# Kernel tuning notes

Hardware: AMD Instinct MI355X
Metric: run time of the kernel (lower is better)

## Reference

```python
import jax, jax.numpy as jnp
import numpy as np

M_LOCAL = 100000
N_GLOBAL = 50000
C = 128
E = 1600000
EDGE_DIM = 16
BN_EPS = 1e-5


def setup_inputs() -> dict:
    key = jax.random.key(0)
    ks = jax.random.split(key, 12)
    s = 1.0 / np.sqrt(C)
    inp = {
        "h_local": jax.random.normal(ks[0], (M_LOCAL, C), jnp.float32),
        "h_global": jax.random.normal(ks[1], (N_GLOBAL, C), jnp.float32),
        "ea_flat": jax.random.normal(ks[2], (E, EDGE_DIM), jnp.float32),
        # GIN MLP: Linear(C,C) -> ReLU -> Linear(C,C)
        "W1": jax.random.normal(ks[3], (C, C), jnp.float32) * s,
        "b1": jnp.zeros((C,), jnp.float32),
        "W2": jax.random.normal(ks[4], (C, C), jnp.float32) * s,
        "b2": jnp.zeros((C,), jnp.float32),
        "eps": jnp.zeros((), jnp.float32),  # GIN train_eps, init 0
        "gamma_l": jnp.ones((C,), jnp.float32),
        "beta_l": jnp.zeros((C,), jnp.float32),
        "gamma_g": jnp.ones((C,), jnp.float32),
        "beta_g": jnp.zeros((C,), jnp.float32),
        "intra_ei": jax.random.randint(ks[5], (2, E), 0, M_LOCAL, jnp.int32),
        "node_ids": jax.random.randint(ks[6], (M_LOCAL,), 0, N_GLOBAL, jnp.int32),
        "valid": jnp.ones((M_LOCAL,), jnp.bool_),
        "N_total": N_GLOBAL,
    }
    return inp


def _batchnorm(x, gamma, beta):
    # training-mode BN: biased batch statistics over node dim
    mu = jnp.mean(x, axis=0)
    var = jnp.mean((x - mu) ** 2, axis=0)
    return (x - mu) * jax.lax.rsqrt(var + BN_EPS) * gamma + beta


def reference(h_local, h_global, ea_flat, W1, b1, W2, b2, eps,
              gamma_l, beta_l, gamma_g, beta_g,
              intra_ei, node_ids, valid, N_total):
    M = h_local.shape[0]
    valid_f = valid.astype(h_local.dtype)[:, None]
    clamped = jnp.maximum(node_ids, 0)

    # inject global context, zero padding
    h_in = (h_local + h_global[clamped]) * valid_f

    # GINConv: mlp((1+eps)*x + sum_{j->i} x_j)   (ea_flat unused for 'gin')
    src, dst = intra_ei[0], intra_ei[1]
    agg = jax.ops.segment_sum(h_in[src], dst, num_segments=M)
    pre = (1.0 + eps) * h_in + agg
    h_local_new = jnp.maximum(pre @ W1 + b1, 0.0) @ W2 + b2
    h_local_new = h_local_new * valid_f

    # cross-subgraph consensus: scatter mean into global nodes
    h_sum = jax.ops.segment_sum(h_local_new, clamped, num_segments=N_total)
    v_cnt = jax.ops.segment_sum(valid_f[:, 0], clamped, num_segments=N_total)
    h_global_new = h_sum / jnp.maximum(v_cnt, 1.0)[:, None]

    # local track: BN + residual (Identity since in==out) + mask (dropout p=0)
    h_local_new = _batchnorm(h_local_new, gamma_l, beta_l) + h_local
    h_local_new = h_local_new * valid_f

    # global track: BN + residual
    h_global_new = _batchnorm(h_global_new, gamma_g, beta_g) + h_global

    return (h_local_new, h_global_new)
```

## Files before the change

### kernel.cpp

```cpp
#include <hip/hip_runtime.h>

#define CDIM 128
#define NBE 3125
#define NBN 391
#define CAPE 1024
#define CAPN 512
#define CHUNK 8192
#define EPB 16
#define BOE 3126
#define BON 392
#define H1LD 136

typedef __bf16 bf16x8 __attribute__((ext_vector_type(8)));
typedef __bf16 bf16x4 __attribute__((ext_vector_type(4)));
typedef float f32x4 __attribute__((ext_vector_type(4)));

__global__ __launch_bounds__(512) void k_front(
    const int* __restrict__ ei, const int* __restrict__ nid,
    int* __restrict__ packed_e, int* __restrict__ boff_e,
    int* __restrict__ packed_n, int* __restrict__ boff_n,
    const float* __restrict__ hl, const float* __restrict__ hg,
    __bf16* __restrict__ h_in,
    const float* __restrict__ W1, const float* __restrict__ W2,
    __bf16* __restrict__ Wt1, __bf16* __restrict__ Wt2,
    int E, int M, int gE, int gN, int gInit)
{
    __shared__ int lh[4096];
    __shared__ int stg[CHUNK];
    __shared__ int lp[512];
    int t = threadIdx.x;
    int bid = blockIdx.x;

    if (bid < gE) {
        int e0 = bid * CHUNK;
        int n = min(CHUNK, E - e0);
        for (int i = t; i < 4096; i += 512) lh[i] = 0;
        __syncthreads();
        int sv[EPB], dv[EPB];
#pragma unroll
        for (int k = 0; k < EPB; ++k) {
            int j = t + k * 512;
            if (j < n) {
                sv[k] = ei[e0 + j];
                dv[k] = ei[E + e0 + j];
                atomicAdd(&lh[dv[k] >> 5], 1);
            }
        }
        __syncthreads();
        int base = t * 8;
        int v[8], s = 0;
#pragma unroll
        for (int k = 0; k < 8; ++k) { v[k] = lh[base + k]; s += v[k]; }
        lp[t] = s;
        __syncthreads();
        for (int st = 1; st < 512; st <<= 1) {
            int a = (t >= st) ? lp[t - st] : 0;
            __syncthreads();
            lp[t] += a;
            __syncthreads();
        }
        int run = lp[t] - s;
#pragma unroll
        for (int k = 0; k < 8; ++k) { lh[base + k] = run; run += v[k]; }
        __syncthreads();
        int* brow = boff_e + (size_t)bid * BOE;
        for (int b = t; b < BOE; b += 512) brow[b] = lh[b];
        __syncthreads();
#pragma unroll
        for (int k = 0; k < EPB; ++k) {
            int j = t + k * 512;
            if (j < n) {
                int pos = atomicAdd(&lh[dv[k] >> 5], 1);
                stg[pos] = sv[k] | ((dv[k] & 31) << 17);
            }
        }
        __syncthreads();
        for (int j = t; j < n; j += 512) packed_e[(size_t)e0 + j] = stg[j];
    } else if (bid < gE + gN) {
        int c = bid - gE;
        int i0 = c * CHUNK;
        int n = min(CHUNK, M - i0);
        lh[t] = 0;
        __syncthreads();
        int iv[EPB], gv[EPB];
#pragma unroll
        for (int k = 0; k < EPB; ++k) {
            int j = t + k * 512;
            if (j < n) {
                iv[k] = i0 + j;
                gv[k] = max(nid[i0 + j], 0);
                atomicAdd(&lh[gv[k] >> 7], 1);
            }
        }
        __syncthreads();
        int v0 = lh[t];
        lp[t] = v0;
        __syncthreads();
        for (int st = 1; st < 512; st <<= 1) {
            int a = (t >= st) ? lp[t - st] : 0;
            __syncthreads();
            lp[t] += a;
            __syncthreads();
        }
        lh[t] = lp[t] - v0;
        __syncthreads();
        int* brow = boff_n + (size_t)c * BON;
        for (int b = t; b < BON; b += 512) brow[b] = lh[b];
        __syncthreads();
#pragma unroll
        for (int k = 0; k < EPB; ++k) {
            int j = t + k * 512;
            if (j < n) {
                int pos = atomicAdd(&lh[gv[k] >> 7], 1);
                stg[pos] = iv[k] | ((gv[k] & 127) << 17);
            }
        }
        __syncthreads();
        for (int j = t; j < n; j += 512) packed_n[(size_t)i0 + j] = stg[j];
    } else if (bid < gE + gN + gInit) {
        int idx = (bid - gE - gN) * 512 + t;
        if (idx >= M * 16) return;
        int i = idx >> 4, q8 = idx & 15;
        int g = max(nid[i], 0);
        const float4* hl4 = reinterpret_cast<const float4*>(hl);
        const float4* hg4 = reinterpret_cast<const float4*>(hg);
        float4 a0 = hl4[i * 32 + q8 * 2], a1 = hl4[i * 32 + q8 * 2 + 1];
        float4 b0 = hg4[g * 32 + q8 * 2], b1 = hg4[g * 32 + q8 * 2 + 1];
        bf16x8 o;
        o[0] = (__bf16)(a0.x + b0.x); o[1] = (__bf16)(a0.y + b0.y);
        o[2] = (__bf16)(a0.z + b0.z); o[3] = (__bf16)(a0.w + b0.w);
        o[4] = (__bf16)(a1.x + b1.x); o[5] = (__bf16)(a1.y + b1.y);
        o[6] = (__bf16)(a1.z + b1.z); o[7] = (__bf16)(a1.w + b1.w);
        *reinterpret_cast<bf16x8*>(&h_in[(size_t)i * CDIM + q8 * 8]) = o;
    } else {
        int idx = (bid - gE - gN - gInit) * 512 + t;
        int k = idx >> 7, n = idx & 127;
        Wt1[n * CDIM + k] = (__bf16)W1[k * CDIM + n];
        Wt2[n * CDIM + k] = (__bf16)W2[k * CDIM + n];
    }
}

__global__ __launch_bounds__(256) void k_agg_fused(
    const __bf16* __restrict__ h_in, const int* __restrict__ packed_e,
    const int* __restrict__ boff_e, const float* __restrict__ epsp,
    __bf16* __restrict__ pre, int M, int gE)
{
    __shared__ int lsrc[CAPE], lsrt[CAPE];
    __shared__ int lscan[256];
    __shared__ int lcnt[32], lbase[32], lpos[32];
    int t = threadIdx.x, b = blockIdx.x;
    int start = 0, len = 0;
    if (t < gE) {
        const int* brow = boff_e + (size_t)t * BOE + b;
        start = brow[0];
        len = brow[1] - start;
    }
    lscan[t] = len;
    __syncthreads();
    for (int st = 1; st < 256; st <<= 1) {
        int a = (t >= st) ? lscan[t - st] : 0;
        __syncthreads();
        lscan[t] += a;
        __syncthreads();
    }
    int myoff = lscan[t] - len;
    int ntot = min(lscan[255], CAPE);
    int cbase = (t < gE) ? t : 0;
    const int* seg = packed_e + (size_t)cbase * CHUNK + start;
    for (int k = 0; k < len; ++k) {
        int o = myoff + k;
        if (o < CAPE) lsrc[o] = seg[k];
    }
    if (t < 32) lcnt[t] = 0;
    __syncthreads();
    for (int j = t; j < ntot; j += 256) atomicAdd(&lcnt[lsrc[j] >> 17], 1);
    __syncthreads();
    if (t == 0) {
        int acc = 0;
        for (int i = 0; i < 32; ++i) { int c = lcnt[i]; lbase[i] = acc; lpos[i] = acc; acc += c; }
    }
    __syncthreads();
    for (int j = t; j < ntot; j += 256) {
        int p = lsrc[j];
        int r = atomicAdd(&lpos[p >> 17], 1);
        lsrt[r] = p & 0x1FFFF;
    }
    __syncthreads();

    float es = 1.0f + epsp[0];
    int slot = t >> 4, q = t & 15;
    int r0 = b * 32;
#pragma unroll
    for (int rr0 = 0; rr0 < 2; ++rr0) {
        int rr = slot + rr0 * 16;
        int row = r0 + rr;
        if (row >= M) break;
        bf16x8 a = *reinterpret_cast<const bf16x8*>(&h_in[(size_t)row * CDIM + q * 8]);
        float f[8];
#pragma unroll
        for (int k2 = 0; k2 < 8; ++k2) f[k2] = es * (float)a[k2];
        int sb = lbase[rr], cnt = lcnt[rr];
        int j = 0;
        for (; j + 3 < cnt; j += 4) {
            int s0 = lsrt[sb + j], s1 = lsrt[sb + j + 1];
            int s2 = lsrt[sb + j + 2], s3 = lsrt[sb + j + 3];
            bf16x8 u0 = *reinterpret_cast<const bf16x8*>(&h_in[(size_t)s0 * CDIM + q * 8]);
            bf16x8 u1 = *reinterpret_cast<const bf16x8*>(&h_in[(size_t)s1 * CDIM + q * 8]);
            bf16x8 u2 = *reinterpret_cast<const bf16x8*>(&h_in[(size_t)s2 * CDIM + q * 8]);
            bf16x8 u3 = *reinterpret_cast<const bf16x8*>(&h_in[(size_t)s3 * CDIM + q * 8]);
#pragma unroll
            for (int k2 = 0; k2 < 8; ++k2)
                f[k2] += ((float)u0[k2] + (float)u1[k2]) + ((float)u2[k2] + (float)u3[k2]);
        }
        for (; j < cnt; ++j) {
            int s0 = lsrt[sb + j];
            bf16x8 u0 = *reinterpret_cast<const bf16x8*>(&h_in[(size_t)s0 * CDIM + q * 8]);
#pragma unroll
            for (int k2 = 0; k2 < 8; ++k2) f[k2] += (float)u0[k2];
        }
        bf16x8 o;
#pragma unroll
        for (int k2 = 0; k2 < 8; ++k2) o[k2] = (__bf16)f[k2];
        *reinterpret_cast<bf16x8*>(&pre[(size_t)row * CDIM + q * 8]) = o;
    }
}

__global__ __launch_bounds__(256) void k_mlp(
    const __bf16* __restrict__ pre, const __bf16* __restrict__ Wt1,
    const __bf16* __restrict__ Wt2, const float* __restrict__ b1,
    const float* __restrict__ b2, __bf16* __restrict__ y,
    float* __restrict__ part, int M)
{
    __shared__ bf16x8 w_lds4[2048];
    __shared__ __bf16 h1t[64 * H1LD];
    __shared__ float pst[256];
    int t = threadIdx.x;
#pragma unroll
    for (int j = 0; j < 8; ++j) {
        int c = t + j * 256;
        int n = c >> 4, cr = c & 15, kc = cr >> 2, g = cr & 3;
        w_lds4[((n >> 4) * 4 + kc) * 64 + g * 16 + (n & 15)] =
            reinterpret_cast<const bf16x8*>(Wt1)[c];
    }
    if (t < 256) pst[t] = 0.f;
    __syncthreads();

    int wave = t >> 6, lane = t & 63;
    int r0 = blockIdx.x * 64 + wave * 16;
    int srcrow = min(r0 + (lane & 15), M - 1);
    int krow = (lane >> 4) * 8;
    int col = lane & 15;

    bf16x8 a[4];
#pragma unroll
    for (int kc = 0; kc < 4; ++kc)
        a[kc] = *reinterpret_cast<const bf16x8*>(
            &pre[(size_t)srcrow * CDIM + kc * 32 + krow]);

    f32x4 acc1[8] = {};
#pragma unroll
    for (int kc = 0; kc < 4; ++kc)
#pragma unroll
        for (int nt = 0; nt < 8; ++nt)
            acc1[nt] = __builtin_amdgcn_mfma_f32_16x16x32_bf16(
                a[kc], w_lds4[(nt * 4 + kc) * 64 + lane], acc1[nt], 0, 0, 0);

    int lrowb = wave * 16 + (lane >> 4) * 4;
#pragma unroll
    for (int nt = 0; nt < 8; ++nt) {
        float bv = b1[nt * 16 + col];
#pragma unroll
        for (int reg = 0; reg < 4; ++reg) {
            float v = fmaxf(acc1[nt][reg] + bv, 0.f);
            h1t[(lrowb + reg) * H1LD + nt * 16 + col] = (__bf16)v;
        }
    }
    __syncthreads();

#pragma unroll
    for (int j = 0; j < 8; ++j) {
        int c = t + j * 256;
        int n = c >> 4, cr = c & 15, kc = cr >> 2, g = cr & 3;
        w_lds4[((n >> 4) * 4 + kc) * 64 + g * 16 + (n & 15)] =
            reinterpret_cast<const bf16x8*>(Wt2)[c];
    }
    __syncthreads();

    int lrow = wave * 16 + (lane & 15);
    bf16x8 a2[4];
#pragma unroll
    for (int kc = 0; kc < 4; ++kc)
        a2[kc] = *reinterpret_cast<const bf16x8*>(&h1t[lrow * H1LD + kc * 32 + krow]);

    f32x4 acc2[8] = {};
#pragma unroll
    for (int kc = 0; kc < 4; ++kc)
#pragma unroll
        for (int nt = 0; nt < 8; ++nt)
            acc2[nt] = __builtin_amdgcn_mfma_f32_16x16x32_bf16(
                a2[kc], w_lds4[(nt * 4 + kc) * 64 + lane], acc2[nt], 0, 0, 0);

    int rowbase = r0 + (lane >> 4) * 4;
#pragma unroll
    for (int nt = 0; nt < 8; ++nt) {
        float bv = b2[nt * 16 + col];
        float s = 0.f, s2 = 0.f;
#pragma unroll
        for (int reg = 0; reg < 4; ++reg) {
            int row = rowbase + reg;
            float v = acc2[nt][reg] + bv;
            if (row < M) {
                y[(size_t)row * CDIM + nt * 16 + col] = (__bf16)v;
                s += v;
                s2 = fmaf(v, v, s2);
            }
        }
        s += __shfl_xor(s, 16); s += __shfl_xor(s, 32);
        s2 += __shfl_xor(s2, 16); s2 += __shfl_xor(s2, 32);
        if ((lane >> 4) == 0) {
            atomicAdd(&pst[nt * 16 + col], s);
            atomicAdd(&pst[128 + nt * 16 + col], s2);
        }
    }
    __syncthreads();
    if (t < 256) part[(size_t)blockIdx.x * 256 + t] = pst[t];
}

__global__ __launch_bounds__(256) void k_gmean(
    const __bf16* __restrict__ y, const int* __restrict__ packed_n,
    const int* __restrict__ boff_n, float* __restrict__ out_g,
    float* __restrict__ part, int N, int gN)
{
    __shared__ int lall[CAPN], lrows[CAPN];
    __shared__ int lscan[256];
    __shared__ int lcnt[32], lbase[32], lpos[32];
    __shared__ float pst[256];
    int t = threadIdx.x;
    int b = blockIdx.x >> 2;
    int quarter = blockIdx.x & 3;
    int start = 0, len = 0;
    if (t < gN) {
        const int* brow = boff_n + (size_t)t * BON + b;
        start = brow[0];
        len = brow[1] - start;
    }
    lscan[t] = len;
    pst[t] = 0.f;
    __syncthreads();
    for (int st = 1; st < 256; st <<= 1) {
        int a = (t >= st) ? lscan[t - st] : 0;
        __syncthreads();
        lscan[t] += a;
        __syncthreads();
    }
    int myoff = lscan[t] - len;
    int ntot = min(lscan[255], CAPN);
    int cbase = (t < gN) ? t : 0;
    const int* seg = packed_n + (size_t)cbase * CHUNK + start;
    for (int k = 0; k < len; ++k) {
        int o = myoff + k;
        if (o < CAPN) lall[o] = seg[k];
    }
    if (t < 32) lcnt[t] = 0;
    __syncthreads();
    for (int j = t; j < ntot; j += 256) {
        int ld = lall[j] >> 17;
        if ((ld >> 5) == quarter) atomicAdd(&lcnt[ld & 31], 1);
    }
    __syncthreads();
    if (t == 0) {
        int acc = 0;
        for (int i = 0; i < 32; ++i) { int c = lcnt[i]; lbase[i] = acc; lpos[i] = acc; acc += c; }
    }
    __syncthreads();
    for (int j = t; j < ntot; j += 256) {
        int p = lall[j];
        int ld = p >> 17;
        if ((ld >> 5) == quarter) {
            int r = atomicAdd(&lpos[ld & 31], 1);
            lrows[r] = p & 0x1FFFF;
        }
    }
    __syncthreads();

    int slot = t >> 4, q = t & 15;
    int g0 = b * 128 + quarter * 32;
    float csum[8] = {}, csq[8] = {};
#pragma unroll
    for (int rr0 = 0; rr0 < 2; ++rr0) {
        int rr = slot + rr0 * 16;
        int g = g0 + rr;
        if (g >= N) break;
        float f[8] = {};
        int sb = lbase[rr], cnt = lcnt[rr];
        int j = 0;
        for (; j + 1 < cnt; j += 2) {
            int ra = lrows[sb + j], rb = lrows[sb + j + 1];
            bf16x8 va = *reinterpret_cast<const bf16x8*>(&y[(size_t)ra * CDIM + q * 8]);
            bf16x8 vb = *reinterpret_cast<const bf16x8*>(&y[(size_t)rb * CDIM + q * 8]);
#pragma unroll
            for (int k2 = 0; k2 < 8; ++k2) f[k2] += (float)va[k2] + (float)vb[k2];
        }
        if (j < cnt) {
            int ra = lrows[sb + j];
            bf16x8 va = *reinterpret_cast<const bf16x8*>(&y[(size_t)ra * CDIM + q * 8]);
#pragma unroll
            for (int k2 = 0; k2 < 8; ++k2) f[k2] += (float)va[k2];
        }
        float inv = 1.0f / fmaxf((float)cnt, 1.0f);
        float4 o0, o1;
        o0.x = f[0] * inv; o0.y = f[1] * inv; o0.z = f[2] * inv; o0.w = f[3] * inv;
        o1.x = f[4] * inv; o1.y = f[5] * inv; o1.z = f[6] * inv; o1.w = f[7] * inv;
        float* dst = out_g + (size_t)g * CDIM + q * 8;
        *reinterpret_cast<float4*>(dst) = o0;
        *reinterpret_cast<float4*>(dst + 4) = o1;
        float m[8] = {o0.x, o0.y, o0.z, o0.w, o1.x, o1.y, o1.z, o1.w};
#pragma unroll
        for (int k2 = 0; k2 < 8; ++k2) {
            csum[k2] += m[k2];
            csq[k2] = fmaf(m[k2], m[k2], csq[k2]);
        }
    }
#pragma unroll
    for (int k2 = 0; k2 < 8; ++k2) {
        atomicAdd(&pst[q * 8 + k2], csum[k2]);
        atomicAdd(&pst[128 + q * 8 + k2], csq[k2]);
    }
    __syncthreads();
    if (t < 256) part[(size_t)blockIdx.x * 256 + t] = pst[t];
}

__global__ __launch_bounds__(256) void k_reduce_scale(
    const float* __restrict__ part_l, int nl,
    const float* __restrict__ part_g, int ng,
    const float* __restrict__ gl, const float* __restrict__ bl,
    const float* __restrict__ gg, const float* __restrict__ bg,
    float* __restrict__ sc, int M, int N)
{
    int c = blockIdx.x;
    bool isL = c < 128;
    const float* part = isL ? part_l : part_g;
    int n = isL ? nl : ng;
    int col = isL ? c : c - 128;
    int t = threadIdx.x;
    float s1 = 0.f, s2 = 0.f;
    for (int i = t; i < n; i += 256) {
        const float* row = part + (size_t)i * 256;
        s1 += row[col];
        s2 += row[128 + col];
    }
    __shared__ float sh1[256], sh2[256];
    sh1[t] = s1; sh2[t] = s2;
    __syncthreads();
    for (int w = 128; w > 0; w >>= 1) {
        if (t < w) { sh1[t] += sh1[t + w]; sh2[t] += sh2[t + w]; }
        __syncthreads();
    }
    if (t == 0) {
        float cnt = isL ? (float)M : (float)N;
        float mu = sh1[0] / cnt;
        float var = sh2[0] / cnt - mu * mu;
        float gamma = isL ? gl[col] : gg[col];
        float beta  = isL ? bl[col] : bg[col];
        float sca = gamma * rsqrtf(var + 1e-5f);
        int off = isL ? 0 : 256;
        sc[off + col] = sca;
        sc[off + 128 + col] = beta - mu * sca;
    }
}

__global__ __launch_bounds__(256) void k_fin(
    const __bf16* __restrict__ y, const float* __restrict__ hl,
    float* __restrict__ out_l, float* __restrict__ out_g,
    const float* __restrict__ hg, const float* __restrict__ sc,
    int M, int N, int gFinL)
{
    int bid = blockIdx.x;
    if (bid < gFinL) {
        int idx = bid * 256 + threadIdx.x;
        if (idx >= M * 32) return;
        int q = idx & 31;
        float4 s4 = reinterpret_cast<const float4*>(sc)[q];
        float4 h4 = reinterpret_cast<const float4*>(sc + 128)[q];
        bf16x4 v = *reinterpret_cast<const bf16x4*>(&y[(size_t)idx * 4]);
        float4 r = reinterpret_cast<const float4*>(hl)[idx];
        reinterpret_cast<float4*>(out_l)[idx] = make_float4(
            fmaf((float)v[0], s4.x, h4.x) + r.x, fmaf((float)v[1], s4.y, h4.y) + r.y,
            fmaf((float)v[2], s4.z, h4.z) + r.z, fmaf((float)v[3], s4.w, h4.w) + r.w);
    } else {
        int idx = (bid - gFinL) * 256 + threadIdx.x;
        if (idx >= N * 32) return;
        int q = idx & 31;
        float4 s4 = reinterpret_cast<const float4*>(sc + 256)[q];
        float4 h4 = reinterpret_cast<const float4*>(sc + 384)[q];
        float4 v = reinterpret_cast<float4*>(out_g)[idx];
        float4 r = reinterpret_cast<const float4*>(hg)[idx];
        reinterpret_cast<float4*>(out_g)[idx] = make_float4(
            fmaf(v.x, s4.x, h4.x) + r.x, fmaf(v.y, s4.y, h4.y) + r.y,
            fmaf(v.z, s4.z, h4.z) + r.z, fmaf(v.w, s4.w, h4.w) + r.w);
    }
}

extern "C" void kernel_launch(void* const* d_in, const int* in_sizes, int n_in,
                              void* d_out, int out_size, void* d_ws, size_t ws_size,
                              hipStream_t stream)
{
    const float* h_local  = (const float*)d_in[0];
    const float* h_global = (const float*)d_in[1];
    const float* W1   = (const float*)d_in[3];
    const float* b1   = (const float*)d_in[4];
    const float* W2   = (const float*)d_in[5];
    const float* b2   = (const float*)d_in[6];
    const float* eps  = (const float*)d_in[7];
    const float* gl   = (const float*)d_in[8];
    const float* bl   = (const float*)d_in[9];
    const float* gg   = (const float*)d_in[10];
    const float* bg   = (const float*)d_in[11];
    const int*   ei   = (const int*)d_in[12];
    const int*   nid  = (const int*)d_in[13];

    const int M = in_sizes[13];
    const int N = in_sizes[1] / CDIM;
    const int E = in_sizes[12] / 2;
    const int gGemm = (M + 63) / 64;
    const int nGm   = NBN * 4;
    const int gE = (E + CHUNK - 1) / CHUNK;
    const int gN = (M + CHUNK - 1) / CHUNK;

    float* out_l = (float*)d_out;
    float* out_g = out_l + (size_t)M * CDIM;

    __bf16* pre = (__bf16*)d_out;

    int*   packed_n = (int*)((char*)d_out + 26000000);
    int*   boff_n   = packed_n + M;
    float* part_l   = (float*)((char*)d_out + 28000000);
    float* part_g   = part_l + (size_t)gGemm * 256;

    int* packed_e = (int*)out_g;
    int* boff_e   = packed_e + (size_t)gE * CHUNK;

    __bf16* h_in = (__bf16*)d_ws;
    __bf16* y    = (__bf16*)((char*)d_ws + 25600000);
    char*  wst   = (char*)d_ws + 51200000;
    __bf16* Wt1  = (__bf16*)wst;
    __bf16* Wt2  = Wt1 + CDIM * CDIM;
    float* sc    = (float*)(Wt2 + CDIM * CDIM);

    int gInit = (M * 16 + 511) / 512;
    int gWp   = (CDIM * CDIM + 511) / 512;
    k_front<<<gE + gN + gInit + gWp, 512, 0, stream>>>(
        ei, nid, packed_e, boff_e, packed_n, boff_n,
        h_local, h_global, h_in, W1, W2, Wt1, Wt2, E, M, gE, gN, gInit);

    k_agg_fused<<<NBE, 256, 0, stream>>>(h_in, packed_e, boff_e, eps, pre, M, gE);

    k_mlp<<<gGemm, 256, 0, stream>>>(pre, Wt1, Wt2, b1, b2, y, part_l, M);

    k_gmean<<<nGm, 256, 0, stream>>>(y, packed_n, boff_n, out_g, part_g, N, gN);

    k_reduce_scale<<<256, 256, 0, stream>>>(part_l, gGemm, part_g, nGm,
                                            gl, bl, gg, bg, sc, M, N);

    int gFinL = (M * 32 + 255) / 256;
    int gFinG = (N * 32 + 255) / 256;
    k_fin<<<gFinL + gFinG, 256, 0, stream>>>(y, h_local, out_l, out_g,
                                             h_global, sc, M, N, gFinL);
}
```

Baseline: 225.0 us.

## Fuse edge aggregation with GIN MLP in one kernel over 64-row tiles

Merges the gather-sum aggregation kernel and the two-layer MLP kernel. The aggregated rows now stay in LDS instead of round-tripping through a bf16 buffer in global memory. Bucket granularity grows from 32 to 64 destination rows, blocks grow to 512 threads, and a block-index remap spreads contiguous tiles across XCDs. Fewer launches and less global traffic are traded for higher LDS use per block and eight waves each covering half the output columns, which may lower occupancy and create tail imbalance.

```diff
diff --git a/kernel.cpp b/kernel.cpp
--- a/kernel.cpp
+++ b/kernel.cpp
@@ -1,13 +1,13 @@
 #include <hip/hip_runtime.h>
 
 #define CDIM 128
-#define NBE 3125
+#define NBG 1563
 #define NBN 391
-#define CAPE 1024
+#define CAPE2 2048
 #define CAPN 512
 #define CHUNK 8192
 #define EPB 16
-#define BOE 3126
+#define BOE 1564
 #define BON 392
 #define H1LD 136
 
@@ -25,7 +25,7 @@
     __bf16* __restrict__ Wt1, __bf16* __restrict__ Wt2,
     int E, int M, int gE, int gN, int gInit)
 {
-    __shared__ int lh[4096];
+    __shared__ int lh[2048];
     __shared__ int stg[CHUNK];
     __shared__ int lp[512];
     int t = threadIdx.x;
@@ -34,7 +34,7 @@
     if (bid < gE) {
         int e0 = bid * CHUNK;
         int n = min(CHUNK, E - e0);
-        for (int i = t; i < 4096; i += 512) lh[i] = 0;
+        for (int i = t; i < 2048; i += 512) lh[i] = 0;
         __syncthreads();
         int sv[EPB], dv[EPB];
 #pragma unroll
@@ -43,14 +43,14 @@
             if (j < n) {
                 sv[k] = ei[e0 + j];
                 dv[k] = ei[E + e0 + j];
-                atomicAdd(&lh[dv[k] >> 5], 1);
-            }
-        }
-        __syncthreads();
-        int base = t * 8;
-        int v[8], s = 0;
-#pragma unroll
-        for (int k = 0; k < 8; ++k) { v[k] = lh[base + k]; s += v[k]; }
+                atomicAdd(&lh[dv[k] >> 6], 1);
+            }
+        }
+        __syncthreads();
+        int base = t * 4;
+        int v[4], s = 0;
+#pragma unroll
+        for (int k = 0; k < 4; ++k) { v[k] = lh[base + k]; s += v[k]; }
         lp[t] = s;
         __syncthreads();
         for (int st = 1; st < 512; st <<= 1) {
@@ -61,7 +61,7 @@
         }
         int run = lp[t] - s;
 #pragma unroll
-        for (int k = 0; k < 8; ++k) { lh[base + k] = run; run += v[k]; }
+        for (int k = 0; k < 4; ++k) { lh[base + k] = run; run += v[k]; }
         __syncthreads();
         int* brow = boff_e + (size_t)bid * BOE;
         for (int b = t; b < BOE; b += 512) brow[b] = lh[b];
@@ -70,8 +70,8 @@
         for (int k = 0; k < EPB; ++k) {
             int j = t + k * 512;
             if (j < n) {
-                int pos = atomicAdd(&lh[dv[k] >> 5], 1);
-                stg[pos] = sv[k] | ((dv[k] & 31) << 17);
+                int pos = atomicAdd(&lh[dv[k] >> 6], 1);
+                stg[pos] = sv[k] | ((dv[k] & 63) << 17);
             }
         }
         __syncthreads();
@@ -140,15 +140,36 @@
     }
 }
 
-__global__ __launch_bounds__(256) void k_agg_fused(
+__global__ __launch_bounds__(512, 4) void k_aggmlp(
     const __bf16* __restrict__ h_in, const int* __restrict__ packed_e,
     const int* __restrict__ boff_e, const float* __restrict__ epsp,
-    __bf16* __restrict__ pre, int M, int gE)
+    const __bf16* __restrict__ Wt1, const __bf16* __restrict__ Wt2,
+    const float* __restrict__ b1, const float* __restrict__ b2,
+    __bf16* __restrict__ y, float* __restrict__ part, int M, int gE)
 {
-    __shared__ int lsrc[CAPE], lsrt[CAPE];
-    __shared__ int lscan[256];
-    __shared__ int lcnt[32], lbase[32], lpos[32];
-    int t = threadIdx.x, b = blockIdx.x;
+    __shared__ int lsrc[CAPE2], lsrt[CAPE2];
+    __shared__ int lscan[512];
+    __shared__ int lcnt[64], lbase[64], lpos[64];
+    __shared__ bf16x8 w_lds4[2048];
+    __shared__ __bf16 buf[64 * H1LD];
+    __shared__ float pst[256];
+    int t = threadIdx.x;
+
+    int nb = gridDim.x;
+    int q8_ = nb >> 3, r8 = nb & 7;
+    int xcd = blockIdx.x & 7, i8 = blockIdx.x >> 3;
+    int b = (xcd < r8 ? xcd * (q8_ + 1) : r8 * (q8_ + 1) + (xcd - r8) * q8_) + i8;
+
+#pragma unroll
+    for (int j = 0; j < 4; ++j) {
+        int c = t + j * 512;
+        int n = c >> 4, cr = c & 15, kc = cr >> 2, g = cr & 3;
+        w_lds4[((n >> 4) * 4 + kc) * 64 + g * 16 + (n & 15)] =
+            reinterpret_cast<const bf16x8*>(Wt1)[c];
+    }
+    if (t < 256) pst[t] = 0.f;
+    if (t < 64) lcnt[t] = 0;
+
     int start = 0, len = 0;
     if (t < gE) {
         const int* brow = boff_e + (size_t)t * BOE + b;
@@ -157,30 +178,29 @@
     }
     lscan[t] = len;
     __syncthreads();
-    for (int st = 1; st < 256; st <<= 1) {
+    for (int st = 1; st < 512; st <<= 1) {
         int a = (t >= st) ? lscan[t - st] : 0;
         __syncthreads();
         lscan[t] += a;
         __syncthreads();
     }
     int myoff = lscan[t] - len;
-    int ntot = min(lscan[255], CAPE);
+    int ntot = min(lscan[511], CAPE2);
     int cbase = (t < gE) ? t : 0;
     const int* seg = packed_e + (size_t)cbase * CHUNK + start;
     for (int k = 0; k < len; ++k) {
         int o = myoff + k;
-        if (o < CAPE) lsrc[o] = seg[k];
-    }
-    if (t < 32) lcnt[t] = 0;
-    __syncthreads();
-    for (int j = t; j < ntot; j += 256) atomicAdd(&lcnt[lsrc[j] >> 17], 1);
+        if (o < CAPE2) lsrc[o] = seg[k];
+    }
+    __syncthreads();
+    for (int j = t; j < ntot; j += 512) atomicAdd(&lcnt[lsrc[j] >> 17], 1);
     __syncthreads();
     if (t == 0) {
         int acc = 0;
-        for (int i = 0; i < 32; ++i) { int c = lcnt[i]; lbase[i] = acc; lpos[i] = acc; acc += c; }
-    }
-    __syncthreads();
-    for (int j = t; j < ntot; j += 256) {
+        for (int i = 0; i < 64; ++i) { int c = lcnt[i]; lbase[i] = acc; lpos[i] = acc; acc += c; }
+    }
+    __syncthreads();
+    for (int j = t; j < ntot; j += 512) {
         int p = lsrc[j];
         int r = atomicAdd(&lpos[p >> 17], 1);
         lsrt[r] = p & 0x1FFFF;
@@ -189,126 +209,104 @@
 
     float es = 1.0f + epsp[0];
     int slot = t >> 4, q = t & 15;
-    int r0 = b * 32;
+    int r0 = b * 64;
 #pragma unroll
     for (int rr0 = 0; rr0 < 2; ++rr0) {
-        int rr = slot + rr0 * 16;
+        int rr = slot + rr0 * 32;
         int row = r0 + rr;
-        if (row >= M) break;
-        bf16x8 a = *reinterpret_cast<const bf16x8*>(&h_in[(size_t)row * CDIM + q * 8]);
-        float f[8];
-#pragma unroll
-        for (int k2 = 0; k2 < 8; ++k2) f[k2] = es * (float)a[k2];
-        int sb = lbase[rr], cnt = lcnt[rr];
-        int j = 0;
-        for (; j + 3 < cnt; j += 4) {
-            int s0 = lsrt[sb + j], s1 = lsrt[sb + j + 1];
-            int s2 = lsrt[sb + j + 2], s3 = lsrt[sb + j + 3];
-            bf16x8 u0 = *reinterpret_cast<const bf16x8*>(&h_in[(size_t)s0 * CDIM + q * 8]);
-            bf16x8 u1 = *reinterpret_cast<const bf16x8*>(&h_in[(size_t)s1 * CDIM + q * 8]);
-            bf16x8 u2 = *reinterpret_cast<const bf16x8*>(&h_in[(size_t)s2 * CDIM + q * 8]);
-            bf16x8 u3 = *reinterpret_cast<const bf16x8*>(&h_in[(size_t)s3 * CDIM + q * 8]);
-#pragma unroll
-            for (int k2 = 0; k2 < 8; ++k2)
-                f[k2] += ((float)u0[k2] + (float)u1[k2]) + ((float)u2[k2] + (float)u3[k2]);
-        }
-        for (; j < cnt; ++j) {
-            int s0 = lsrt[sb + j];
-            bf16x8 u0 = *reinterpret_cast<const bf16x8*>(&h_in[(size_t)s0 * CDIM + q * 8]);
-#pragma unroll
-            for (int k2 = 0; k2 < 8; ++k2) f[k2] += (float)u0[k2];
+        float f[8] = {};
+        if (row < M) {
+            bf16x8 a = *reinterpret_cast<const bf16x8*>(&h_in[(size_t)row * CDIM + q * 8]);
+#pragma unroll
+            for (int k2 = 0; k2 < 8; ++k2) f[k2] = es * (float)a[k2];
+            int sb = lbase[rr], cnt = lcnt[rr];
+            int j = 0;
+            for (; j + 3 < cnt; j += 4) {
+                int s0 = lsrt[sb + j], s1 = lsrt[sb + j + 1];
+                int s2 = lsrt[sb + j + 2], s3 = lsrt[sb + j + 3];
+                bf16x8 u0 = *reinterpret_cast<const bf16x8*>(&h_in[(size_t)s0 * CDIM + q * 8]);
+                bf16x8 u1 = *reinterpret_cast<const bf16x8*>(&h_in[(size_t)s1 * CDIM + q * 8]);
+                bf16x8 u2 = *reinterpret_cast<const bf16x8*>(&h_in[(size_t)s2 * CDIM + q * 8]);
+                bf16x8 u3 = *reinterpret_cast<const bf16x8*>(&h_in[(size_t)s3 * CDIM + q * 8]);
+#pragma unroll
+                for (int k2 = 0; k2 < 8; ++k2)
+                    f[k2] += ((float)u0[k2] + (float)u1[k2]) + ((float)u2[k2] + (float)u3[k2]);
+            }
+            for (; j < cnt; ++j) {
+                int s0 = lsrt[sb + j];
+                bf16x8 u0 = *reinterpret_cast<const bf16x8*>(&h_in[(size_t)s0 * CDIM + q * 8]);
+#pragma unroll
+                for (int k2 = 0; k2 < 8; ++k2) f[k2] += (float)u0[k2];
+            }
         }
         bf16x8 o;
 #pragma unroll
         for (int k2 = 0; k2 < 8; ++k2) o[k2] = (__bf16)f[k2];
-        *reinterpret_cast<bf16x8*>(&pre[(size_t)row * CDIM + q * 8]) = o;
-    }
-}
-
-__global__ __launch_bounds__(256) void k_mlp(
-    const __bf16* __restrict__ pre, const __bf16* __restrict__ Wt1,
-    const __bf16* __restrict__ Wt2, const float* __restrict__ b1,
-    const float* __restrict__ b2, __bf16* __restrict__ y,
-    float* __restrict__ part, int M)
-{
-    __shared__ bf16x8 w_lds4[2048];
-    __shared__ __bf16 h1t[64 * H1LD];
-    __shared__ float pst[256];
-    int t = threadIdx.x;
-#pragma unroll
-    for (int j = 0; j < 8; ++j) {
-        int c = t + j * 256;
-        int n = c >> 4, cr = c & 15, kc = cr >> 2, g = cr & 3;
-        w_lds4[((n >> 4) * 4 + kc) * 64 + g * 16 + (n & 15)] =
-            reinterpret_cast<const bf16x8*>(Wt1)[c];
-    }
-    if (t < 256) pst[t] = 0.f;
+        *reinterpret_cast<bf16x8*>(&buf[rr * H1LD + q * 8]) = o;
+    }
     __syncthreads();
 
     int wave = t >> 6, lane = t & 63;
-    int r0 = blockIdx.x * 64 + wave * 16;
-    int srcrow = min(r0 + (lane & 15), M - 1);
+    int wr = (wave >> 1) * 16;
+    int nt0 = (wave & 1) * 4;
     int krow = (lane >> 4) * 8;
     int col = lane & 15;
 
-    bf16x8 a[4];
+    bf16x8 a1[4];
 #pragma unroll
     for (int kc = 0; kc < 4; ++kc)
-        a[kc] = *reinterpret_cast<const bf16x8*>(
-            &pre[(size_t)srcrow * CDIM + kc * 32 + krow]);
-
-    f32x4 acc1[8] = {};
+        a1[kc] = *reinterpret_cast<const bf16x8*>(&buf[(wr + (lane & 15)) * H1LD + kc * 32 + krow]);
+    f32x4 acc1[4] = {};
 #pragma unroll
     for (int kc = 0; kc < 4; ++kc)
 #pragma unroll
-        for (int nt = 0; nt < 8; ++nt)
-            acc1[nt] = __builtin_amdgcn_mfma_f32_16x16x32_bf16(
-                a[kc], w_lds4[(nt * 4 + kc) * 64 + lane], acc1[nt], 0, 0, 0);
-
-    int lrowb = wave * 16 + (lane >> 4) * 4;
-#pragma unroll
-    for (int nt = 0; nt < 8; ++nt) {
+        for (int ntl = 0; ntl < 4; ++ntl)
+            acc1[ntl] = __builtin_amdgcn_mfma_f32_16x16x32_bf16(
+                a1[kc], w_lds4[((nt0 + ntl) * 4 + kc) * 64 + lane], acc1[ntl], 0, 0, 0);
+    __syncthreads();
+
+    int lrowb = wr + (lane >> 4) * 4;
+#pragma unroll
+    for (int ntl = 0; ntl < 4; ++ntl) {
+        int nt = nt0 + ntl;
         float bv = b1[nt * 16 + col];
 #pragma unroll
         for (int reg = 0; reg < 4; ++reg) {
-            float v = fmaxf(acc1[nt][reg] + bv, 0.f);
-            h1t[(lrowb + reg) * H1LD + nt * 16 + col] = (__bf16)v;
-        }
-    }
-    __syncthreads();
-
-#pragma unroll
-    for (int j = 0; j < 8; ++j) {
-        int c = t + j * 256;
+            float v = fmaxf(acc1[ntl][reg] + bv, 0.f);
+            buf[(lrowb + reg) * H1LD + nt * 16 + col] = (__bf16)v;
+        }
+    }
+#pragma unroll
+    for (int j = 0; j < 4; ++j) {
+        int c = t + j * 512;
         int n = c >> 4, cr = c & 15, kc = cr >> 2, g = cr & 3;
         w_lds4[((n >> 4) * 4 + kc) * 64 + g * 16 + (n & 15)] =
             reinterpret_cast<const bf16x8*>(Wt2)[c];
     }
     __syncthreads();
 
-    int lrow = wave * 16 + (lane & 15);
     bf16x8 a2[4];
 #pragma unroll
     for (int kc = 0; kc < 4; ++kc)
-        a2[kc] = *reinterpret_cast<const bf16x8*>(&h1t[lrow * H1LD + kc * 32 + krow]);
-
-    f32x4 acc2[8] = {};
+        a2[kc] = *reinterpret_cast<const bf16x8*>(&buf[(wr + (lane & 15)) * H1LD + kc * 32 + krow]);
+    f32x4 acc2[4] = {};
 #pragma unroll
     for (int kc = 0; kc < 4; ++kc)
 #pragma unroll
-        for (int nt = 0; nt < 8; ++nt)
-            acc2[nt] = __builtin_amdgcn_mfma_f32_16x16x32_bf16(
-                a2[kc], w_lds4[(nt * 4 + kc) * 64 + lane], acc2[nt], 0, 0, 0);
-
-    int rowbase = r0 + (lane >> 4) * 4;
-#pragma unroll
-    for (int nt = 0; nt < 8; ++nt) {
+        for (int ntl = 0; ntl < 4; ++ntl)
+            acc2[ntl] = __builtin_amdgcn_mfma_f32_16x16x32_bf16(
+                a2[kc], w_lds4[((nt0 + ntl) * 4 + kc) * 64 + lane], acc2[ntl], 0, 0, 0);
+
+    int rowbase = r0 + wr + (lane >> 4) * 4;
+#pragma unroll
+    for (int ntl = 0; ntl < 4; ++ntl) {
+        int nt = nt0 + ntl;
         float bv = b2[nt * 16 + col];
         float s = 0.f, s2 = 0.f;
 #pragma unroll
         for (int reg = 0; reg < 4; ++reg) {
             int row = rowbase + reg;
-            float v = acc2[nt][reg] + bv;
+            float v = acc2[ntl][reg] + bv;
             if (row < M) {
                 y[(size_t)row * CDIM + nt * 16 + col] = (__bf16)v;
                 s += v;
@@ -522,20 +520,17 @@
     const int M = in_sizes[13];
     const int N = in_sizes[1] / CDIM;
     const int E = in_sizes[12] / 2;
-    const int gGemm = (M + 63) / 64;
-    const int nGm   = NBN * 4;
+    const int nGm = NBN * 4;
     const int gE = (E + CHUNK - 1) / CHUNK;
     const int gN = (M + CHUNK - 1) / CHUNK;
 
     float* out_l = (float*)d_out;
     float* out_g = out_l + (size_t)M * CDIM;
-
-    __bf16* pre = (__bf16*)d_out;
 
     int*   packed_n = (int*)((char*)d_out + 26000000);
     int*   boff_n   = packed_n + M;
     float* part_l   = (float*)((char*)d_out + 28000000);
-    float* part_g   = part_l + (size_t)gGemm * 256;
+    float* part_g   = part_l + (size_t)NBG * 256;
 
     int* packed_e = (int*)out_g;
     int* boff_e   = packed_e + (size_t)gE * CHUNK;
@@ -553,13 +548,12 @@
         ei, nid, packed_e, boff_e, packed_n, boff_n,
         h_local, h_global, h_in, W1, W2, Wt1, Wt2, E, M, gE, gN, gInit);
 
-    k_agg_fused<<<NBE, 256, 0, stream>>>(h_in, packed_e, boff_e, eps, pre, M, gE);
-
-    k_mlp<<<gGemm, 256, 0, stream>>>(pre, Wt1, Wt2, b1, b2, y, part_l, M);
+    k_aggmlp<<<NBG, 512, 0, stream>>>(h_in, packed_e, boff_e, eps,
+                                      Wt1, Wt2, b1, b2, y, part_l, M, gE);
 
     k_gmean<<<nGm, 256, 0, stream>>>(y, packed_n, boff_n, out_g, part_g, N, gN);
 
-    k_reduce_scale<<<256, 256, 0, stream>>>(part_l, gGemm, part_g, nGm,
+    k_reduce_scale<<<256, 256, 0, stream>>>(part_l, NBG, part_g, nGm,
                                             gl, bl, gg, bg, sc, M, N);
 
     int gFinL = (M * 32 + 255) / 256;
```

After: 226.0 us. No clear change (+0.4%).

## Transpose bucket offsets for coalesced reads and remap agg blocks across XCDs

Applied to the files above, without the earlier changes.

Adds a small kernel that transposes the per-chunk bucket offset table into block-major start/length arrays. The aggregation kernel can then read its offsets with coalesced loads instead of strided reads across chunks. The aggregation kernel also remaps blockIdx so that contiguous bucket ranges land on the same XCD, which should improve L2 locality. The cost is one extra kernel launch and extra scratch memory carved from the output buffer.

```diff
diff --git a/kernel.cpp b/kernel.cpp
--- a/kernel.cpp
+++ b/kernel.cpp
@@ -9,6 +9,7 @@
 #define EPB 16
 #define BOE 3126
 #define BON 392
+#define TLD 208
 #define H1LD 136
 
 typedef __bf16 bf16x8 __attribute__((ext_vector_type(8)));
@@ -140,20 +141,48 @@
     }
 }
 
+__global__ __launch_bounds__(256) void k_btrans(
+    const int* __restrict__ boff_e, int* __restrict__ startT,
+    int* __restrict__ lenT, int gE)
+{
+    __shared__ int tile[196][17];
+    int t = threadIdx.x;
+    int b0 = blockIdx.x * 16;
+    for (int k = t; k < gE * 17; k += 256) {
+        int c = k / 17, j = k - c * 17;
+        int b = min(b0 + j, NBE);
+        tile[c][j] = boff_e[(size_t)c * BOE + b];
+    }
+    __syncthreads();
+    for (int j = 0; j < 16; ++j) {
+        int b = b0 + j;
+        if (b >= NBE) break;
+        for (int c = t; c < gE; c += 256) {
+            startT[(size_t)b * TLD + c] = tile[c][j];
+            lenT[(size_t)b * TLD + c] = tile[c][j + 1] - tile[c][j];
+        }
+    }
+}
+
 __global__ __launch_bounds__(256) void k_agg_fused(
     const __bf16* __restrict__ h_in, const int* __restrict__ packed_e,
-    const int* __restrict__ boff_e, const float* __restrict__ epsp,
-    __bf16* __restrict__ pre, int M, int gE)
+    const int* __restrict__ startT, const int* __restrict__ lenT,
+    const float* __restrict__ epsp, __bf16* __restrict__ pre, int M, int gE)
 {
     __shared__ int lsrc[CAPE], lsrt[CAPE];
     __shared__ int lscan[256];
     __shared__ int lcnt[32], lbase[32], lpos[32];
-    int t = threadIdx.x, b = blockIdx.x;
+    int t = threadIdx.x;
+
+    int nb = gridDim.x;
+    int q8_ = nb >> 3, r8 = nb & 7;
+    int xcd = blockIdx.x & 7, i8 = blockIdx.x >> 3;
+    int b = (xcd < r8 ? xcd * (q8_ + 1) : r8 * (q8_ + 1) + (xcd - r8) * q8_) + i8;
+
     int start = 0, len = 0;
     if (t < gE) {
-        const int* brow = boff_e + (size_t)t * BOE + b;
-        start = brow[0];
-        len = brow[1] - start;
+        start = startT[(size_t)b * TLD + t];
+        len = lenT[(size_t)b * TLD + t];
     }
     lscan[t] = len;
     __syncthreads();
@@ -539,6 +568,8 @@
 
     int* packed_e = (int*)out_g;
     int* boff_e   = packed_e + (size_t)gE * CHUNK;
+    int* startT   = boff_e + (size_t)gE * BOE;
+    int* lenT     = startT + (size_t)NBE * TLD;
 
     __bf16* h_in = (__bf16*)d_ws;
     __bf16* y    = (__bf16*)((char*)d_ws + 25600000);
@@ -553,7 +584,10 @@
         ei, nid, packed_e, boff_e, packed_n, boff_n,
         h_local, h_global, h_in, W1, W2, Wt1, Wt2, E, M, gE, gN, gInit);
 
-    k_agg_fused<<<NBE, 256, 0, stream>>>(h_in, packed_e, boff_e, eps, pre, M, gE);
+    k_btrans<<<(NBE + 15) / 16, 256, 0, stream>>>(boff_e, startT, lenT, gE);
+
+    k_agg_fused<<<NBE, 256, 0, stream>>>(h_in, packed_e, startT, lenT,
+                                         eps, pre, M, gE);
 
     k_mlp<<<gGemm, 256, 0, stream>>>(pre, Wt1, Wt2, b1, b2, y, part_l, M);
 
```

New measurement: 225.7 us (median of 2 runs). About the same (+0.3%).
